# Kernel optimization log

Hardware: AMD Instinct MI355X
Metric: run time of the kernel (lower is better)

## Reference

```python
import jax, jax.numpy as jnp
import numpy as np

N = 50000      # num_nodes
E = 800000     # num_edges
D = 128        # hidden_dim
V = 32000      # vocab_size
T = 8          # num_edge_types
NT = 16        # num_node_types


def setup_inputs() -> dict:
    key = jax.random.key(0)
    ks = jax.random.split(key, 10)
    s = 1.0 / np.sqrt(D)
    return {
        "x": jax.random.randint(ks[0], (N,), 0, V),
        "edge_index": jax.random.randint(ks[1], (2, E), 0, N),
        "edge_type": jax.random.randint(ks[2], (E,), 0, T),
        "node_type": jax.random.randint(ks[3], (N,), 0, NT),
        "emb": jax.random.normal(ks[4], (V, D), dtype=jnp.float32) * s,
        "W_rel": jax.random.normal(ks[5], (T, D, D), dtype=jnp.float32) * s,
        "b_node": jax.random.normal(ks[6], (NT, D), dtype=jnp.float32) * 0.01,
        "W_ih": jax.random.normal(ks[7], (3 * D, D), dtype=jnp.float32) * s,
        "W_hh": jax.random.normal(ks[8], (3 * D, D), dtype=jnp.float32) * s,
        "b_ih": jnp.zeros((3 * D,), dtype=jnp.float32),
        "b_hh": jnp.zeros((3 * D,), dtype=jnp.float32),
    }


def _gru_cell(inp, h, W_ih, W_hh, b_ih, b_hh):
    # torch.nn.GRUCell semantics
    gi = inp @ W_ih.T + b_ih   # [N, 3D]
    gh = h @ W_hh.T + b_hh     # [N, 3D]
    i_r, i_z, i_n = jnp.split(gi, 3, axis=-1)
    h_r, h_z, h_n = jnp.split(gh, 3, axis=-1)
    r = jax.nn.sigmoid(i_r + h_r)
    z = jax.nn.sigmoid(i_z + h_z)
    n = jnp.tanh(i_n + r * h_n)
    return (1.0 - z) * n + z * h


def reference(x, edge_index, edge_type, node_type, emb, W_rel, b_node, W_ih, W_hh, b_ih, b_hh):
    h = emb[x]                                   # [N, D] node embeddings
    src, dst = edge_index[0], edge_index[1]
    n_nodes = h.shape[0]
    for _ in range(5):
        # relational message passing: per-edge-type linear on source nodes
        Ht = jnp.einsum('nd,tdf->ntf', h, W_rel)  # [N, T, D] all-type transforms
        msg = Ht[src, edge_type]                  # [E, D] gather per edge
        aggr = jax.ops.segment_sum(msg, dst, num_segments=n_nodes)  # scatter-add to dst
        aggr = aggr + b_node[node_type]           # node-type-specific bias
        h = _gru_cell(aggr, h, W_ih, W_hh, b_ih, b_hh)
    return h
```

## Files before the change

### kernel.cpp

```cpp
#include <hip/hip_runtime.h>
#include <hip/hip_fp16.h>
#include <math.h>

#define N_NODES 50000
#define N_EDGES 800000
#define D 128
#define T_TYPES 8
#define TPAD 136
#define NBLK_SCAN 196

typedef short short8 __attribute__((ext_vector_type(8)));
typedef float float4v __attribute__((ext_vector_type(4)));
typedef unsigned short ushort_t;

static __device__ __forceinline__ unsigned short f2bf(float f) {
    unsigned u = __float_as_uint(f);
    u += 0x7fff + ((u >> 16) & 1);
    return (unsigned short)(u >> 16);
}
static __device__ __forceinline__ float bf2f(unsigned short b) {
    return __uint_as_float((unsigned)b << 16);
}
static __device__ __forceinline__ void splitbf(float x, unsigned short& hi, unsigned short& lo) {
    unsigned short h_ = f2bf(x);
    hi = h_;
    lo = f2bf(x - bf2f(h_));
}

__global__ void embed_gather(const int* __restrict__ x, const float* __restrict__ emb,
                             ushort_t* __restrict__ hhi, ushort_t* __restrict__ hlo) {
    int n = blockIdx.x;
    int d = threadIdx.x;
    float v = emb[(size_t)x[n] * D + d];
    unsigned short a, b;
    splitbf(v, a, b);
    hhi[(size_t)n * D + d] = a;
    hlo[(size_t)n * D + d] = b;
}

__global__ void convert_wrelT(const float* __restrict__ Wrel,
                              ushort_t* __restrict__ hi, ushort_t* __restrict__ lo) {
    int idx = blockIdx.x * 256 + threadIdx.x;
    int t = idx >> 14;
    int rem = idx & 16383;
    int f = rem >> 7;
    int d = rem & 127;
    unsigned short a, b;
    splitbf(Wrel[((size_t)t << 14) + (d << 7) + f], a, b);
    hi[idx] = a;
    lo[idx] = b;
}

__global__ void convert_w(const float* __restrict__ in,
                          ushort_t* __restrict__ hi, ushort_t* __restrict__ lo, int n) {
    int idx = blockIdx.x * 256 + threadIdx.x;
    if (idx < n) {
        unsigned short a, b;
        splitbf(in[idx], a, b);
        hi[idx] = a;
        lo[idx] = b;
    }
}

__global__ void count_deg(const int* __restrict__ ei, int* __restrict__ deg) {
    int e = blockIdx.x * 256 + threadIdx.x;
    if (e >= N_EDGES) return;
    atomicAdd(&deg[ei[N_EDGES + e]], 1);
}

__global__ __launch_bounds__(256) void scan_blocks(const int* __restrict__ deg,
                                                   int* __restrict__ bsums) {
    __shared__ int red[4];
    int idx = blockIdx.x * 256 + threadIdx.x;
    int v = (idx < N_NODES) ? deg[idx] : 0;
#pragma unroll
    for (int o = 32; o > 0; o >>= 1) v += __shfl_down(v, o);
    if ((threadIdx.x & 63) == 0) red[threadIdx.x >> 6] = v;
    __syncthreads();
    if (threadIdx.x == 0) bsums[blockIdx.x] = red[0] + red[1] + red[2] + red[3];
}

__global__ __launch_bounds__(256) void scan_tops(int* __restrict__ bsums) {
    __shared__ int s[256];
    int tid = threadIdx.x;
    int v = (tid < NBLK_SCAN) ? bsums[tid] : 0;
    s[tid] = v;
    __syncthreads();
#pragma unroll
    for (int o = 1; o < 256; o <<= 1) {
        int u = (tid >= o) ? s[tid - o] : 0;
        __syncthreads();
        s[tid] += u;
        __syncthreads();
    }
    if (tid < NBLK_SCAN) bsums[tid] = s[tid] - v;
}

__global__ __launch_bounds__(256) void scan_final(const int* __restrict__ bsums,
                                                  int* __restrict__ deg_cursor,
                                                  int* __restrict__ rs) {
    __shared__ int s[256];
    int tid = threadIdx.x;
    int idx = blockIdx.x * 256 + tid;
    int v = (idx < N_NODES) ? deg_cursor[idx] : 0;
    s[tid] = v;
    __syncthreads();
#pragma unroll
    for (int o = 1; o < 256; o <<= 1) {
        int u = (tid >= o) ? s[tid - o] : 0;
        __syncthreads();
        s[tid] += u;
        __syncthreads();
    }
    int excl = s[tid] - v + bsums[blockIdx.x];
    if (idx < N_NODES) {
        rs[idx] = excl;
        deg_cursor[idx] = excl;
    }
    if (idx == 0) rs[N_NODES] = N_EDGES;
}

__global__ void fill_csr(const int* __restrict__ ei, const int* __restrict__ et,
                         int* __restrict__ cursor, int* __restrict__ packed) {
    int e = blockIdx.x * 256 + threadIdx.x;
    if (e >= N_EDGES) return;
    int dst = ei[N_EDGES + e];
    int pos = atomicAdd(&cursor[dst], 1);
    packed[pos] = (ei[e] << 3) | et[e];
}

__global__ __launch_bounds__(256, 2) void gemm_rel(const ushort_t* __restrict__ hhi,
                                                   const ushort_t* __restrict__ hlo,
                                                   const ushort_t* __restrict__ Whi,
                                                   const ushort_t* __restrict__ Wlo,
                                                   ushort_t* __restrict__ Ht) {
    __shared__ __align__(16) ushort_t wlds[2][128 * TPAD];
    const int tid = threadIdx.x;
    const int wave = tid >> 6, lane = tid & 63;
    const int q = lane >> 4, li = lane & 15;
    const int t = blockIdx.y;
    const int m_base = blockIdx.x * 128 + wave * 32;

    {
        const ushort_t* gh = Whi + ((size_t)t << 14);
        const ushort_t* gl = Wlo + ((size_t)t << 14);
#pragma unroll
        for (int i = 0; i < 8; ++i) {
            int g = (i * 256 + tid) * 8;
            int row = g >> 7, col = g & 127;
            *(short8*)(&wlds[0][row * TPAD + col]) = *(const short8*)(gh + g);
            *(short8*)(&wlds[1][row * TPAD + col]) = *(const short8*)(gl + g);
        }
    }
    __syncthreads();

    int r0 = m_base + li;      if (r0 > N_NODES - 1) r0 = N_NODES - 1;
    int r1 = m_base + 16 + li; if (r1 > N_NODES - 1) r1 = N_NODES - 1;
    const ushort_t* A0h = hhi + (size_t)r0 * D + q * 8;
    const ushort_t* A0l = hlo + (size_t)r0 * D + q * 8;
    const ushort_t* A1h = hhi + (size_t)r1 * D + q * 8;
    const ushort_t* A1l = hlo + (size_t)r1 * D + q * 8;

    short8 a0h[4], a0l[4], a1h[4], a1l[4];
#pragma unroll
    for (int ks = 0; ks < 4; ++ks) {
        a0h[ks] = *(const short8*)(A0h + ks * 32);
        a0l[ks] = *(const short8*)(A0l + ks * 32);
        a1h[ks] = *(const short8*)(A1h + ks * 32);
        a1l[ks] = *(const short8*)(A1l + ks * 32);
    }

    float4v acc[2][8];
#pragma unroll
    for (int m = 0; m < 2; ++m)
#pragma unroll
        for (int ft = 0; ft < 8; ++ft) acc[m][ft] = (float4v){0.f, 0.f, 0.f, 0.f};

#pragma unroll
    for (int ks = 0; ks < 4; ++ks) {
#pragma unroll
        for (int ft = 0; ft < 8; ++ft) {
            const int lo_off = (ft * 16 + li) * TPAD + ks * 32 + q * 8;
            short8 bh = *(const short8*)(&wlds[0][lo_off]);
            short8 bl = *(const short8*)(&wlds[1][lo_off]);
            acc[0][ft] = __builtin_amdgcn_mfma_f32_16x16x32_bf16(a0h[ks], bh, acc[0][ft], 0, 0, 0);
            acc[0][ft] = __builtin_amdgcn_mfma_f32_16x16x32_bf16(a0l[ks], bh, acc[0][ft], 0, 0, 0);
            acc[0][ft] = __builtin_amdgcn_mfma_f32_16x16x32_bf16(a0h[ks], bl, acc[0][ft], 0, 0, 0);
            acc[1][ft] = __builtin_amdgcn_mfma_f32_16x16x32_bf16(a1h[ks], bh, acc[1][ft], 0, 0, 0);
            acc[1][ft] = __builtin_amdgcn_mfma_f32_16x16x32_bf16(a1l[ks], bh, acc[1][ft], 0, 0, 0);
            acc[1][ft] = __builtin_amdgcn_mfma_f32_16x16x32_bf16(a1h[ks], bl, acc[1][ft], 0, 0, 0);
        }
    }

    __syncthreads();
    ushort_t* tw = &wlds[0][0] + wave * 32 * TPAD;
#pragma unroll
    for (int m = 0; m < 2; ++m)
#pragma unroll
        for (int ft = 0; ft < 8; ++ft)
#pragma unroll
            for (int r = 0; r < 4; ++r) {
                __half hv = __float2half_rn(acc[m][ft][r]);
                tw[(m * 16 + q * 4 + r) * TPAD + ft * 16 + li] = __half_as_ushort(hv);
            }
#pragma unroll
    for (int i = 0; i < 8; ++i) {
        int row = i * 4 + q;
        int col = li * 8;
        short8 v = *(const short8*)(tw + row * TPAD + col);
        int orow = m_base + row;
        if (orow < N_NODES)
            *(short8*)(Ht + (size_t)orow * 1024 + (t << 7) + col) = v;
    }
}

__global__ __launch_bounds__(256) void aggregate_csr(const int* __restrict__ rs,
                                                     const int* __restrict__ packed,
                                                     const ushort_t* __restrict__ Ht,
                                                     const int* __restrict__ nt,
                                                     const float* __restrict__ b_node,
                                                     ushort_t* __restrict__ ahi,
                                                     ushort_t* __restrict__ alo) {
    int n = blockIdx.x * 4 + (threadIdx.x >> 6);
    if (n >= N_NODES) return;
    const int lane = threadIdx.x & 63;
    const int beg = rs[n], end = rs[n + 1];
    const __half2* Ht2 = (const __half2*)Ht;

    float2 acc = ((const float2*)(b_node + (size_t)nt[n] * D))[lane];

    int i = beg;
    for (; i + 3 < end; i += 4) {
        int p0 = packed[i], p1 = packed[i + 1], p2 = packed[i + 2], p3 = packed[i + 3];
        float2 f0 = __half22float2(Ht2[(size_t)p0 * 64 + lane]);
        float2 f1 = __half22float2(Ht2[(size_t)p1 * 64 + lane]);
        float2 f2 = __half22float2(Ht2[(size_t)p2 * 64 + lane]);
        float2 f3 = __half22float2(Ht2[(size_t)p3 * 64 + lane]);
        acc.x += (f0.x + f1.x) + (f2.x + f3.x);
        acc.y += (f0.y + f1.y) + (f2.y + f3.y);
    }
    for (; i < end; ++i) {
        int pk = packed[i];
        float2 fv = __half22float2(Ht2[(size_t)pk * 64 + lane]);
        acc.x += fv.x;
        acc.y += fv.y;
    }

    unsigned short h0, l0, h1, l1;
    splitbf(acc.x, h0, l0);
    splitbf(acc.y, h1, l1);
    ((unsigned*)ahi)[(size_t)n * 64 + lane] = (unsigned)h0 | ((unsigned)h1 << 16);
    ((unsigned*)alo)[(size_t)n * 64 + lane] = (unsigned)l0 | ((unsigned)l1 << 16);
}

__global__ __launch_bounds__(512, 4) void gru_mfma(const ushort_t* __restrict__ ahi,
                                                   const ushort_t* __restrict__ alo,
                                                   ushort_t* __restrict__ hhi,
                                                   ushort_t* __restrict__ hlo,
                                                   const ushort_t* __restrict__ Wihi,
                                                   const ushort_t* __restrict__ Wilo,
                                                   const ushort_t* __restrict__ Whhi,
                                                   const ushort_t* __restrict__ Whlo,
                                                   const float* __restrict__ b_ih,
                                                   const float* __restrict__ b_hh,
                                                   float* __restrict__ h,
                                                   int write_h) {
    __shared__ __align__(16) ushort_t xlds[4][32 * TPAD];
    const int tid = threadIdx.x;
    const int wave = tid >> 6, lane = tid & 63;
    const int q = lane >> 4, li = lane & 15;
    const int n0 = blockIdx.x * 32;
    const int f = wave * 16 + li;

    {
        int g = tid * 8;
        int row = g >> 7, col = g & 127;
        int gr = n0 + row;
        if (gr > N_NODES - 1) gr = N_NODES - 1;
        size_t go = (size_t)gr * D + col;
        int la = row * TPAD + col;
        *(short8*)(&xlds[0][la]) = *(const short8*)(ahi + go);
        *(short8*)(&xlds[1][la]) = *(const short8*)(alo + go);
        *(short8*)(&xlds[2][la]) = *(const short8*)(hhi + go);
        *(short8*)(&xlds[3][la]) = *(const short8*)(hlo + go);
    }
    __syncthreads();

    const size_t oR = (size_t)f * D + q * 8;
    const size_t oZ = (size_t)(D + f) * D + q * 8;
    const size_t oN = (size_t)(2 * D + f) * D + q * 8;

    float4v aR[2], aZ[2], aI[2], aH[2];
#pragma unroll
    for (int m = 0; m < 2; ++m) {
        aR[m] = (float4v){0.f, 0.f, 0.f, 0.f};
        aZ[m] = aR[m]; aI[m] = aR[m]; aH[m] = aR[m];
    }

#pragma unroll
    for (int ks = 0; ks < 4; ++ks) {
        const int off = ks * 32;
        short8 wIRh = *(const short8*)(Wihi + oR + off);
        short8 wIRl = *(const short8*)(Wilo + oR + off);
        short8 wHRh = *(const short8*)(Whhi + oR + off);
        short8 wHRl = *(const short8*)(Whlo + oR + off);
        short8 wIZh = *(const short8*)(Wihi + oZ + off);
        short8 wIZl = *(const short8*)(Wilo + oZ + off);
        short8 wHZh = *(const short8*)(Whhi + oZ + off);
        short8 wHZl = *(const short8*)(Whlo + oZ + off);
        short8 wINh = *(const short8*)(Wihi + oN + off);
        short8 wINl = *(const short8*)(Wilo + oN + off);
        short8 wHNh = *(const short8*)(Whhi + oN + off);
        short8 wHNl = *(const short8*)(Whlo + oN + off);
#pragma unroll
        for (int m = 0; m < 2; ++m) {
            const int lo_off = (m * 16 + li) * TPAD + off + q * 8;
            short8 xah = *(const short8*)(&xlds[0][lo_off]);
            short8 xal = *(const short8*)(&xlds[1][lo_off]);
            short8 xhh = *(const short8*)(&xlds[2][lo_off]);
            short8 xhl = *(const short8*)(&xlds[3][lo_off]);
            aR[m] = __builtin_amdgcn_mfma_f32_16x16x32_bf16(xah, wIRh, aR[m], 0, 0, 0);
            aR[m] = __builtin_amdgcn_mfma_f32_16x16x32_bf16(xal, wIRh, aR[m], 0, 0, 0);
            aR[m] = __builtin_amdgcn_mfma_f32_16x16x32_bf16(xah, wIRl, aR[m], 0, 0, 0);
            aR[m] = __builtin_amdgcn_mfma_f32_16x16x32_bf16(xhh, wHRh, aR[m], 0, 0, 0);
            aR[m] = __builtin_amdgcn_mfma_f32_16x16x32_bf16(xhl, wHRh, aR[m], 0, 0, 0);
            aR[m] = __builtin_amdgcn_mfma_f32_16x16x32_bf16(xhh, wHRl, aR[m], 0, 0, 0);
            aZ[m] = __builtin_amdgcn_mfma_f32_16x16x32_bf16(xah, wIZh, aZ[m], 0, 0, 0);
            aZ[m] = __builtin_amdgcn_mfma_f32_16x16x32_bf16(xal, wIZh, aZ[m], 0, 0, 0);
            aZ[m] = __builtin_amdgcn_mfma_f32_16x16x32_bf16(xah, wIZl, aZ[m], 0, 0, 0);
            aZ[m] = __builtin_amdgcn_mfma_f32_16x16x32_bf16(xhh, wHZh, aZ[m], 0, 0, 0);
            aZ[m] = __builtin_amdgcn_mfma_f32_16x16x32_bf16(xhl, wHZh, aZ[m], 0, 0, 0);
            aZ[m] = __builtin_amdgcn_mfma_f32_16x16x32_bf16(xhh, wHZl, aZ[m], 0, 0, 0);
            aI[m] = __builtin_amdgcn_mfma_f32_16x16x32_bf16(xah, wINh, aI[m], 0, 0, 0);
            aI[m] = __builtin_amdgcn_mfma_f32_16x16x32_bf16(xal, wINh, aI[m], 0, 0, 0);
            aI[m] = __builtin_amdgcn_mfma_f32_16x16x32_bf16(xah, wINl, aI[m], 0, 0, 0);
            aH[m] = __builtin_amdgcn_mfma_f32_16x16x32_bf16(xhh, wHNh, aH[m], 0, 0, 0);
            aH[m] = __builtin_amdgcn_mfma_f32_16x16x32_bf16(xhl, wHNh, aH[m], 0, 0, 0);
            aH[m] = __builtin_amdgcn_mfma_f32_16x16x32_bf16(xhh, wHNl, aH[m], 0, 0, 0);
        }
    }

    const float bR = b_ih[f] + b_hh[f];
    const float bZ = b_ih[D + f] + b_hh[D + f];
    const float bIn = b_ih[2 * D + f];
    const float bHn = b_hh[2 * D + f];

#pragma unroll
    for (int m = 0; m < 2; ++m) {
#pragma unroll
        for (int r = 0; r < 4; ++r) {
            int row = m * 16 + q * 4 + r;
            int node = n0 + row;
            if (node < N_NODES) {
                float hold = bf2f(xlds[2][row * TPAD + f]) + bf2f(xlds[3][row * TPAD + f]);
                float rg = 1.0f / (1.0f + __expf(-(aR[m][r] + bR)));
                float zg = 1.0f / (1.0f + __expf(-(aZ[m][r] + bZ)));
                float narg = aI[m][r] + bIn + rg * (aH[m][r] + bHn);
                float ex = __expf(2.0f * narg);
                float ng = 1.0f - 2.0f / (ex + 1.0f);
                float hn = (1.0f - zg) * ng + zg * hold;
                if (write_h) h[(size_t)node * D + f] = hn;
                unsigned short sh, sl;
                splitbf(hn, sh, sl);
                hhi[(size_t)node * D + f] = sh;
                hlo[(size_t)node * D + f] = sl;
            }
        }
    }
}

extern "C" void kernel_launch(void* const* d_in, const int* in_sizes, int n_in,
                              void* d_out, int out_size, void* d_ws, size_t ws_size,
                              hipStream_t stream) {
    const int* x      = (const int*)d_in[0];
    const int* ei     = (const int*)d_in[1];
    const int* et     = (const int*)d_in[2];
    const int* nt     = (const int*)d_in[3];
    const float* emb  = (const float*)d_in[4];
    const float* Wrel = (const float*)d_in[5];
    const float* b_node = (const float*)d_in[6];
    const float* W_ih = (const float*)d_in[7];
    const float* W_hh = (const float*)d_in[8];
    const float* b_ih = (const float*)d_in[9];
    const float* b_hh = (const float*)d_in[10];

    float* h = (float*)d_out;
    float* ws = (float*)d_ws;

    ushort_t* Ht = (ushort_t*)ws;
    ushort_t* us = (ushort_t*)(ws + 25600000);
    ushort_t* ahi  = us;
    ushort_t* alo  = us + 6400000;
    ushort_t* hhi  = us + 12800000;
    ushort_t* hlo  = us + 19200000;
    ushort_t* Whi  = us + 25600000;
    ushort_t* Wlo  = Whi + 131072;
    ushort_t* Wihi = Wlo + 131072;
    ushort_t* Wilo = Wihi + 49152;
    ushort_t* Whhi = Wilo + 49152;
    ushort_t* Whlo = Whhi + 49152;
    int* rs     = (int*)(ws + 38629376);
    int* packed = rs + 50004;
    int* bsums  = packed + 800000;
    int* deg    = (int*)ws;

    convert_wrelT<<<512, 256, 0, stream>>>(Wrel, Whi, Wlo);
    convert_w<<<192, 256, 0, stream>>>(W_ih, Wihi, Wilo, 3 * D * D);
    convert_w<<<192, 256, 0, stream>>>(W_hh, Whhi, Whlo, 3 * D * D);
    embed_gather<<<N_NODES, 128, 0, stream>>>(x, emb, hhi, hlo);

    hipMemsetAsync(deg, 0, 50000 * sizeof(int), stream);
    count_deg<<<3125, 256, 0, stream>>>(ei, deg);
    scan_blocks<<<NBLK_SCAN, 256, 0, stream>>>(deg, bsums);
    scan_tops<<<1, 256, 0, stream>>>(bsums);
    scan_final<<<NBLK_SCAN, 256, 0, stream>>>(bsums, deg, rs);
    fill_csr<<<3125, 256, 0, stream>>>(ei, et, deg, packed);

    for (int it = 0; it < 5; ++it) {
        dim3 g(391, T_TYPES);
        gemm_rel<<<g, 256, 0, stream>>>(hhi, hlo, Whi, Wlo, Ht);
        aggregate_csr<<<12500, 256, 0, stream>>>(rs, packed, Ht, nt, b_node, ahi, alo);
        gru_mfma<<<1563, 512, 0, stream>>>(ahi, alo, hhi, hlo,
                                           Wihi, Wilo, Whhi, Whlo, b_ih, b_hh,
                                           h, it == 4 ? 1 : 0);
    }
}
```

Baseline: 1.117 ms.

## Make GRU kernel persistent with register-resident weights and double-buffered async loads

Replaces the one-tile-per-block GRU kernel with a persistent kernel of 512 blocks. Each block keeps one half of the GRU weight columns in registers and loops over node tiles. The next tile's inputs are prefetched into LDS with global_load_lds using an XOR-swizzled layout, and outputs are staged through LDS so they are written as coalesced 16-byte stores. Because blocks now read neighbouring rows across tiles, hidden state ping-pongs between two buffers. The aim is to stop reloading weights for every tile and to overlap global loads with MFMA work, at the cost of heavy register pressure and only 256 threads per block.

```diff
diff --git a/kernel.cpp b/kernel.cpp
--- a/kernel.cpp
+++ b/kernel.cpp
@@ -8,6 +8,7 @@
 #define T_TYPES 8
 #define TPAD 136
 #define NBLK_SCAN 196
+#define TILES 1563
 
 typedef short short8 __attribute__((ext_vector_type(8)));
 typedef float float4v __attribute__((ext_vector_type(4)));
@@ -26,6 +27,10 @@
     hi = h_;
     lo = f2bf(x - bf2f(h_));
 }
+
+#define GLOAD16(gp, lp) __builtin_amdgcn_global_load_lds( \
+    (const __attribute__((address_space(1))) unsigned int*)(gp), \
+    (__attribute__((address_space(3))) unsigned int*)(lp), 16, 0, 0)
 
 __global__ void embed_gather(const int* __restrict__ x, const float* __restrict__ emb,
                              ushort_t* __restrict__ hhi, ushort_t* __restrict__ hlo) {
@@ -253,119 +258,170 @@
     ((unsigned*)alo)[(size_t)n * 64 + lane] = (unsigned)l0 | ((unsigned)l1 << 16);
 }
 
-__global__ __launch_bounds__(512, 4) void gru_mfma(const ushort_t* __restrict__ ahi,
-                                                   const ushort_t* __restrict__ alo,
-                                                   ushort_t* __restrict__ hhi,
-                                                   ushort_t* __restrict__ hlo,
-                                                   const ushort_t* __restrict__ Wihi,
-                                                   const ushort_t* __restrict__ Wilo,
-                                                   const ushort_t* __restrict__ Whhi,
-                                                   const ushort_t* __restrict__ Whlo,
-                                                   const float* __restrict__ b_ih,
-                                                   const float* __restrict__ b_hh,
-                                                   float* __restrict__ h,
-                                                   int write_h) {
-    __shared__ __align__(16) ushort_t xlds[4][32 * TPAD];
+__global__ __launch_bounds__(256, 1) void gru_persist(
+    const ushort_t* __restrict__ ahi, const ushort_t* __restrict__ alo,
+    const ushort_t* __restrict__ hhi_in, const ushort_t* __restrict__ hlo_in,
+    ushort_t* __restrict__ hhi_out, ushort_t* __restrict__ hlo_out,
+    const ushort_t* __restrict__ Wihi, const ushort_t* __restrict__ Wilo,
+    const ushort_t* __restrict__ Whhi, const ushort_t* __restrict__ Whlo,
+    const float* __restrict__ b_ih, const float* __restrict__ b_hh,
+    float* __restrict__ h, int write_h)
+{
+    __shared__ __align__(16) ushort_t xlds[2 * 4 * 4096];
+    __shared__ __align__(16) ushort_t tbuf[2][32 * 72];
+
     const int tid = threadIdx.x;
     const int wave = tid >> 6, lane = tid & 63;
     const int q = lane >> 4, li = lane & 15;
-    const int n0 = blockIdx.x * 32;
-    const int f = wave * 16 + li;
-
-    {
-        int g = tid * 8;
-        int row = g >> 7, col = g & 127;
-        int gr = n0 + row;
-        if (gr > N_NODES - 1) gr = N_NODES - 1;
-        size_t go = (size_t)gr * D + col;
-        int la = row * TPAD + col;
-        *(short8*)(&xlds[0][la]) = *(const short8*)(ahi + go);
-        *(short8*)(&xlds[1][la]) = *(const short8*)(alo + go);
-        *(short8*)(&xlds[2][la]) = *(const short8*)(hhi + go);
-        *(short8*)(&xlds[3][la]) = *(const short8*)(hlo + go);
-    }
-    __syncthreads();
-
-    const size_t oR = (size_t)f * D + q * 8;
-    const size_t oZ = (size_t)(D + f) * D + q * 8;
-    const size_t oN = (size_t)(2 * D + f) * D + q * 8;
-
-    float4v aR[2], aZ[2], aI[2], aH[2];
-#pragma unroll
-    for (int m = 0; m < 2; ++m) {
-        aR[m] = (float4v){0.f, 0.f, 0.f, 0.f};
-        aZ[m] = aR[m]; aI[m] = aR[m]; aH[m] = aR[m];
-    }
-
+    const int bid = blockIdx.x;
+    const int fhalf = (bid & 15) >> 3;
+    const int s = (bid >> 4) * 8 + (bid & 7);
+    const int fl = wave * 16 + li;
+    const int fg = fhalf * 64 + fl;
+
+    const size_t oR = (size_t)fg * D + q * 8;
+    const size_t oZ = (size_t)(D + fg) * D + q * 8;
+    const size_t oN = (size_t)(2 * D + fg) * D + q * 8;
+    short8 Wr[12][4];
 #pragma unroll
     for (int ks = 0; ks < 4; ++ks) {
         const int off = ks * 32;
-        short8 wIRh = *(const short8*)(Wihi + oR + off);
-        short8 wIRl = *(const short8*)(Wilo + oR + off);
-        short8 wHRh = *(const short8*)(Whhi + oR + off);
-        short8 wHRl = *(const short8*)(Whlo + oR + off);
-        short8 wIZh = *(const short8*)(Wihi + oZ + off);
-        short8 wIZl = *(const short8*)(Wilo + oZ + off);
-        short8 wHZh = *(const short8*)(Whhi + oZ + off);
-        short8 wHZl = *(const short8*)(Whlo + oZ + off);
-        short8 wINh = *(const short8*)(Wihi + oN + off);
-        short8 wINl = *(const short8*)(Wilo + oN + off);
-        short8 wHNh = *(const short8*)(Whhi + oN + off);
-        short8 wHNl = *(const short8*)(Whlo + oN + off);
+        Wr[0][ks]  = *(const short8*)(Wihi + oR + off);
+        Wr[1][ks]  = *(const short8*)(Wilo + oR + off);
+        Wr[2][ks]  = *(const short8*)(Whhi + oR + off);
+        Wr[3][ks]  = *(const short8*)(Whlo + oR + off);
+        Wr[4][ks]  = *(const short8*)(Wihi + oZ + off);
+        Wr[5][ks]  = *(const short8*)(Wilo + oZ + off);
+        Wr[6][ks]  = *(const short8*)(Whhi + oZ + off);
+        Wr[7][ks]  = *(const short8*)(Whlo + oZ + off);
+        Wr[8][ks]  = *(const short8*)(Wihi + oN + off);
+        Wr[9][ks]  = *(const short8*)(Wilo + oN + off);
+        Wr[10][ks] = *(const short8*)(Whhi + oN + off);
+        Wr[11][ks] = *(const short8*)(Whlo + oN + off);
+    }
+    const float bR  = b_ih[fg] + b_hh[fg];
+    const float bZ  = b_ih[D + fg] + b_hh[D + fg];
+    const float bIn = b_ih[2 * D + fg];
+    const float bHn = b_hh[2 * D + fg];
+
+    const int lrow_base = wave * 4 + (lane >> 4);
+    const int cswz = (lane & 15) ^ (lrow_base & 7);
+
+    {
+#pragma unroll
+        for (int it = 0; it < 2; ++it) {
+            int gr = s * 32 + it * 16 + lrow_base;
+            if (gr > N_NODES - 1) gr = N_NODES - 1;
+            const size_t so = (size_t)gr * D + cswz * 8;
+            ushort_t* l0 = &xlds[(it * 16 + wave * 4) * 128];
+            GLOAD16(ahi + so,    l0);
+            GLOAD16(alo + so,    l0 + 4096);
+            GLOAD16(hhi_in + so, l0 + 8192);
+            GLOAD16(hlo_in + so, l0 + 12288);
+        }
+    }
+    __syncthreads();
+
+    int cur = 0;
+    for (int tile = s; tile < TILES; tile += 256) {
+        const int nxt = tile + 256;
+        if (nxt < TILES) {
+            ushort_t* nb = &xlds[(cur ^ 1) * 16384];
+#pragma unroll
+            for (int it = 0; it < 2; ++it) {
+                int gr = nxt * 32 + it * 16 + lrow_base;
+                if (gr > N_NODES - 1) gr = N_NODES - 1;
+                const size_t so = (size_t)gr * D + cswz * 8;
+                ushort_t* l0 = nb + (it * 16 + wave * 4) * 128;
+                GLOAD16(ahi + so,    l0);
+                GLOAD16(alo + so,    l0 + 4096);
+                GLOAD16(hhi_in + so, l0 + 8192);
+                GLOAD16(hlo_in + so, l0 + 12288);
+            }
+        }
+
+        const ushort_t* xb = &xlds[cur * 16384];
+        float4v aR[2], aZ[2], aI[2], aH[2];
 #pragma unroll
         for (int m = 0; m < 2; ++m) {
-            const int lo_off = (m * 16 + li) * TPAD + off + q * 8;
-            short8 xah = *(const short8*)(&xlds[0][lo_off]);
-            short8 xal = *(const short8*)(&xlds[1][lo_off]);
-            short8 xhh = *(const short8*)(&xlds[2][lo_off]);
-            short8 xhl = *(const short8*)(&xlds[3][lo_off]);
-            aR[m] = __builtin_amdgcn_mfma_f32_16x16x32_bf16(xah, wIRh, aR[m], 0, 0, 0);
-            aR[m] = __builtin_amdgcn_mfma_f32_16x16x32_bf16(xal, wIRh, aR[m], 0, 0, 0);
-            aR[m] = __builtin_amdgcn_mfma_f32_16x16x32_bf16(xah, wIRl, aR[m], 0, 0, 0);
-            aR[m] = __builtin_amdgcn_mfma_f32_16x16x32_bf16(xhh, wHRh, aR[m], 0, 0, 0);
-            aR[m] = __builtin_amdgcn_mfma_f32_16x16x32_bf16(xhl, wHRh, aR[m], 0, 0, 0);
-            aR[m] = __builtin_amdgcn_mfma_f32_16x16x32_bf16(xhh, wHRl, aR[m], 0, 0, 0);
-            aZ[m] = __builtin_amdgcn_mfma_f32_16x16x32_bf16(xah, wIZh, aZ[m], 0, 0, 0);
-            aZ[m] = __builtin_amdgcn_mfma_f32_16x16x32_bf16(xal, wIZh, aZ[m], 0, 0, 0);
-            aZ[m] = __builtin_amdgcn_mfma_f32_16x16x32_bf16(xah, wIZl, aZ[m], 0, 0, 0);
-            aZ[m] = __builtin_amdgcn_mfma_f32_16x16x32_bf16(xhh, wHZh, aZ[m], 0, 0, 0);
-            aZ[m] = __builtin_amdgcn_mfma_f32_16x16x32_bf16(xhl, wHZh, aZ[m], 0, 0, 0);
-            aZ[m] = __builtin_amdgcn_mfma_f32_16x16x32_bf16(xhh, wHZl, aZ[m], 0, 0, 0);
-            aI[m] = __builtin_amdgcn_mfma_f32_16x16x32_bf16(xah, wINh, aI[m], 0, 0, 0);
-            aI[m] = __builtin_amdgcn_mfma_f32_16x16x32_bf16(xal, wINh, aI[m], 0, 0, 0);
-            aI[m] = __builtin_amdgcn_mfma_f32_16x16x32_bf16(xah, wINl, aI[m], 0, 0, 0);
-            aH[m] = __builtin_amdgcn_mfma_f32_16x16x32_bf16(xhh, wHNh, aH[m], 0, 0, 0);
-            aH[m] = __builtin_amdgcn_mfma_f32_16x16x32_bf16(xhl, wHNh, aH[m], 0, 0, 0);
-            aH[m] = __builtin_amdgcn_mfma_f32_16x16x32_bf16(xhh, wHNl, aH[m], 0, 0, 0);
-        }
-    }
-
-    const float bR = b_ih[f] + b_hh[f];
-    const float bZ = b_ih[D + f] + b_hh[D + f];
-    const float bIn = b_ih[2 * D + f];
-    const float bHn = b_hh[2 * D + f];
-
-#pragma unroll
-    for (int m = 0; m < 2; ++m) {
-#pragma unroll
-        for (int r = 0; r < 4; ++r) {
-            int row = m * 16 + q * 4 + r;
-            int node = n0 + row;
-            if (node < N_NODES) {
-                float hold = bf2f(xlds[2][row * TPAD + f]) + bf2f(xlds[3][row * TPAD + f]);
+            aR[m] = (float4v){0.f, 0.f, 0.f, 0.f};
+            aZ[m] = aR[m]; aI[m] = aR[m]; aH[m] = aR[m];
+        }
+#pragma unroll
+        for (int ks = 0; ks < 4; ++ks) {
+#pragma unroll
+            for (int m = 0; m < 2; ++m) {
+                const int row = m * 16 + li;
+                const int inoff = row * 128 + ((ks * 32 + q * 8) ^ ((row & 7) << 3));
+                short8 xah = *(const short8*)(xb + inoff);
+                short8 xal = *(const short8*)(xb + 4096 + inoff);
+                short8 xhh = *(const short8*)(xb + 8192 + inoff);
+                short8 xhl = *(const short8*)(xb + 12288 + inoff);
+                aR[m] = __builtin_amdgcn_mfma_f32_16x16x32_bf16(xah, Wr[0][ks], aR[m], 0, 0, 0);
+                aR[m] = __builtin_amdgcn_mfma_f32_16x16x32_bf16(xal, Wr[0][ks], aR[m], 0, 0, 0);
+                aR[m] = __builtin_amdgcn_mfma_f32_16x16x32_bf16(xah, Wr[1][ks], aR[m], 0, 0, 0);
+                aR[m] = __builtin_amdgcn_mfma_f32_16x16x32_bf16(xhh, Wr[2][ks], aR[m], 0, 0, 0);
+                aR[m] = __builtin_amdgcn_mfma_f32_16x16x32_bf16(xhl, Wr[2][ks], aR[m], 0, 0, 0);
+                aR[m] = __builtin_amdgcn_mfma_f32_16x16x32_bf16(xhh, Wr[3][ks], aR[m], 0, 0, 0);
+                aZ[m] = __builtin_amdgcn_mfma_f32_16x16x32_bf16(xah, Wr[4][ks], aZ[m], 0, 0, 0);
+                aZ[m] = __builtin_amdgcn_mfma_f32_16x16x32_bf16(xal, Wr[4][ks], aZ[m], 0, 0, 0);
+                aZ[m] = __builtin_amdgcn_mfma_f32_16x16x32_bf16(xah, Wr[5][ks], aZ[m], 0, 0, 0);
+                aZ[m] = __builtin_amdgcn_mfma_f32_16x16x32_bf16(xhh, Wr[6][ks], aZ[m], 0, 0, 0);
+                aZ[m] = __builtin_amdgcn_mfma_f32_16x16x32_bf16(xhl, Wr[6][ks], aZ[m], 0, 0, 0);
+                aZ[m] = __builtin_amdgcn_mfma_f32_16x16x32_bf16(xhh, Wr[7][ks], aZ[m], 0, 0, 0);
+                aI[m] = __builtin_amdgcn_mfma_f32_16x16x32_bf16(xah, Wr[8][ks], aI[m], 0, 0, 0);
+                aI[m] = __builtin_amdgcn_mfma_f32_16x16x32_bf16(xal, Wr[8][ks], aI[m], 0, 0, 0);
+                aI[m] = __builtin_amdgcn_mfma_f32_16x16x32_bf16(xah, Wr[9][ks], aI[m], 0, 0, 0);
+                aH[m] = __builtin_amdgcn_mfma_f32_16x16x32_bf16(xhh, Wr[10][ks], aH[m], 0, 0, 0);
+                aH[m] = __builtin_amdgcn_mfma_f32_16x16x32_bf16(xhl, Wr[10][ks], aH[m], 0, 0, 0);
+                aH[m] = __builtin_amdgcn_mfma_f32_16x16x32_bf16(xhh, Wr[11][ks], aH[m], 0, 0, 0);
+            }
+        }
+
+#pragma unroll
+        for (int m = 0; m < 2; ++m) {
+#pragma unroll
+            for (int r = 0; r < 4; ++r) {
+                const int row = m * 16 + q * 4 + r;
+                const int hoff = row * 128 + (fg ^ ((row & 7) << 3));
+                float hold = bf2f(xb[8192 + hoff]) + bf2f(xb[12288 + hoff]);
                 float rg = 1.0f / (1.0f + __expf(-(aR[m][r] + bR)));
                 float zg = 1.0f / (1.0f + __expf(-(aZ[m][r] + bZ)));
                 float narg = aI[m][r] + bIn + rg * (aH[m][r] + bHn);
                 float ex = __expf(2.0f * narg);
                 float ng = 1.0f - 2.0f / (ex + 1.0f);
                 float hn = (1.0f - zg) * ng + zg * hold;
-                if (write_h) h[(size_t)node * D + f] = hn;
                 unsigned short sh, sl;
                 splitbf(hn, sh, sl);
-                hhi[(size_t)node * D + f] = sh;
-                hlo[(size_t)node * D + f] = sl;
+                tbuf[0][row * 72 + fl] = sh;
+                tbuf[1][row * 72 + fl] = sl;
             }
         }
+        __syncthreads();
+
+        {
+            const int row = tid >> 3, col = (tid & 7) * 8;
+            const int node = tile * 32 + row;
+            if (node < N_NODES) {
+                short8 vh = *(const short8*)(&tbuf[0][row * 72 + col]);
+                short8 vl = *(const short8*)(&tbuf[1][row * 72 + col]);
+                const size_t go = (size_t)node * D + fhalf * 64 + col;
+                *(short8*)(hhi_out + go) = vh;
+                *(short8*)(hlo_out + go) = vl;
+                if (write_h) {
+                    float4v f0, f1;
+#pragma unroll
+                    for (int k2 = 0; k2 < 4; ++k2) {
+                        f0[k2] = bf2f((unsigned short)vh[k2]) + bf2f((unsigned short)vl[k2]);
+                        f1[k2] = bf2f((unsigned short)vh[4 + k2]) + bf2f((unsigned short)vl[4 + k2]);
+                    }
+                    *(float4v*)(h + go) = f0;
+                    *(float4v*)(h + go + 4) = f1;
+                }
+            }
+        }
+        __syncthreads();
+        cur ^= 1;
     }
 }
 
@@ -402,6 +458,8 @@
     int* rs     = (int*)(ws + 38629376);
     int* packed = rs + 50004;
     int* bsums  = packed + 800000;
+    ushort_t* hhi2 = (ushort_t*)(ws + 39479808);
+    ushort_t* hlo2 = hhi2 + 6400000;
     int* deg    = (int*)ws;
 
     convert_wrelT<<<512, 256, 0, stream>>>(Wrel, Whi, Wlo);
@@ -417,11 +475,15 @@
     fill_csr<<<3125, 256, 0, stream>>>(ei, et, deg, packed);
 
     for (int it = 0; it < 5; ++it) {
+        const ushort_t* hi_in = (it & 1) ? hhi2 : hhi;
+        const ushort_t* lo_in = (it & 1) ? hlo2 : hlo;
+        ushort_t* hi_out = (it & 1) ? hhi : hhi2;
+        ushort_t* lo_out = (it & 1) ? hlo : hlo2;
         dim3 g(391, T_TYPES);
-        gemm_rel<<<g, 256, 0, stream>>>(hhi, hlo, Whi, Wlo, Ht);
+        gemm_rel<<<g, 256, 0, stream>>>(hi_in, lo_in, Whi, Wlo, Ht);
         aggregate_csr<<<12500, 256, 0, stream>>>(rs, packed, Ht, nt, b_node, ahi, alo);
-        gru_mfma<<<1563, 512, 0, stream>>>(ahi, alo, hhi, hlo,
-                                           Wihi, Wilo, Whhi, Whlo, b_ih, b_hh,
-                                           h, it == 4 ? 1 : 0);
-    }
-}
+        gru_persist<<<512, 256, 0, stream>>>(ahi, alo, hi_in, lo_in, hi_out, lo_out,
+                                             Wihi, Wilo, Whhi, Whlo, b_ih, b_hh,
+                                             h, it == 4 ? 1 : 0);
+    }
+}
```

After: 977.5 us. 1.14x faster.
